# Kernel optimization log

Hardware: AMD Instinct MI355X
Metric: run time of the kernel (lower is better)

The kernel has to match this reference:

```python
import jax, jax.numpy as jnp
import numpy as np

DEPTH = 6
N_LEAF = 2 ** DEPTH          # 64
GATE_COUNT = N_LEAF - 1      # 63
IN_F = 512
OUT_F = 512
BATCH = 1024


def setup_inputs() -> dict:
    key = jax.random.key(0)
    k1, k2, k3 = jax.random.split(key, 3)
    x = jax.random.normal(k1, (BATCH, IN_F), dtype=jnp.float32)
    gw = jax.random.normal(k2, (IN_F, GATE_COUNT), dtype=jnp.float32)
    gb = jnp.zeros((GATE_COUNT,), dtype=jnp.float32)
    pw = jax.random.normal(k3, (OUT_F, IN_F, N_LEAF), dtype=jnp.float32)
    pb = jnp.zeros((OUT_F, N_LEAF), dtype=jnp.float32)
    return {"x": x, "gw": gw, "gb": gb, "pw": pw, "pb": pb}


def _leaf_probs(x, gw, gb, depth):
    # gatings: sigmoid(x @ gw + gb), shape [B, gate_count]
    g = jax.nn.sigmoid(x @ gw + gb)
    B = x.shape[0]
    dens = jnp.ones((B, 1), dtype=x.dtype)  # root density
    offset = 0
    for d in range(depth):
        n = 2 ** d
        gp = g[:, offset:offset + n]                    # parent gatings [B, n]
        # left child multiplies by g, right child by (1 - g), interleaved
        pair = jnp.stack([gp, 1.0 - gp], axis=-1).reshape(B, 2 * n)
        dens = jnp.repeat(dens, 2, axis=1) * pair        # [B, 2n]
        offset += n
    return dens  # [B, n_leaf]


def reference(x, gw, gb, pw, pb):
    leaf = _leaf_probs(x, gw, gb, DEPTH)                 # [B, L]
    # per-leaf linear projections, then mix with leaf probabilities
    y = jnp.einsum('bi,oil->bol', x, pw)                 # [B, O, L]
    out = jnp.einsum('bol,bl->bo', y, leaf) + leaf @ pb.T
    return out
```

## Files before the change

### kernel.cpp

```cpp
#include <hip/hip_runtime.h>
#include <hip/hip_bf16.h>

#define TDEPTH 6
#define NLEAF 64
#define NGATE 63
#define INF 512
#define OUTF 512
#define BATCH 1024

#define BM 256
#define BN 64
#define SPLITK 16
#define THREADS 256
#define KCH 513
#define XN 32

typedef __attribute__((ext_vector_type(4)))  float f32x4;
typedef __attribute__((ext_vector_type(16))) float f32x16;
typedef __attribute__((ext_vector_type(8)))  __bf16 bf16x8;

__global__ __launch_bounds__(256) void leaf_kernel(
    const float* __restrict__ x, const float* __restrict__ gw,
    const float* __restrict__ gb, float* __restrict__ leaf) {
  const int wid = threadIdx.x >> 6, lane = threadIdx.x & 63;
  const int b = blockIdx.x * 4 + wid;
  __shared__ float g[4][NLEAF];
  if (lane < NGATE) {
    const float* xr = x + (size_t)b * INF;
    float a0 = 0.f, a1 = 0.f, a2 = 0.f, a3 = 0.f;
    #pragma unroll 4
    for (int i = 0; i < INF; i += 4) {
      a0 += xr[i + 0] * gw[(i + 0) * NGATE + lane];
      a1 += xr[i + 1] * gw[(i + 1) * NGATE + lane];
      a2 += xr[i + 2] * gw[(i + 2) * NGATE + lane];
      a3 += xr[i + 3] * gw[(i + 3) * NGATE + lane];
    }
    float t = (a0 + a1) + (a2 + a3) + gb[lane];
    g[wid][lane] = 1.0f / (1.0f + __expf(-t));
  }
  __syncthreads();
  float p = 1.0f;
  #pragma unroll
  for (int d = 0; d < TDEPTH; d++) {
    int prefix = lane >> (TDEPTH - 1 - d);
    int node = (1 << d) - 1 + (prefix >> 1);
    float gv = g[wid][node];
    p *= (prefix & 1) ? (1.0f - gv) : gv;
  }
  leaf[(size_t)b * NLEAF + lane] = p;
}

__device__ __forceinline__ void gload_lds16(const void* g, void* l) {
  __builtin_amdgcn_global_load_lds(
      (const __attribute__((address_space(1))) void*)g,
      (__attribute__((address_space(3))) void*)l, 16, 0, 0);
}

__global__ __launch_bounds__(THREADS, 2) void gemm_kernel(
    const float* __restrict__ x, const float* __restrict__ pw,
    const float* __restrict__ pb, const float* __restrict__ leaf,
    float* __restrict__ partial) {
  __shared__ __align__(16) unsigned char Bsm[3][BN * 256];
  __shared__ __align__(16) __bf16 xsm[XN * BM];

  const int tid = threadIdx.x, lane = tid & 63, w = tid >> 6;
  const int lo = lane & 31, half = lane >> 5;

  const int L = (blockIdx.x & 7) * 64 + (blockIdx.x >> 3);
  const int mb = L & 3;
  const int rest = L >> 2;
  const int nb = rest & 7, s = rest >> 3;
  const int m0 = mb * BM, n0 = nb * BN;
  const int cs = XN * s;
  const int nreal = XN;
  const int total = XN + ((s == SPLITK - 1) ? 1 : 0);

  f32x4 lf[2][4][2];
  #pragma unroll
  for (int mr = 0; mr < 2; mr++) {
    const float* lr = leaf + (size_t)(m0 + w * 64 + mr * 32 + lo) * NLEAF + half * 8;
    #pragma unroll
    for (int t4 = 0; t4 < 4; t4++) {
      lf[mr][t4][0] = *(const f32x4*)(lr + t4 * 16);
      lf[mr][t4][1] = *(const f32x4*)(lr + t4 * 16 + 4);
    }
  }

  {
    const float* src = x + (size_t)(m0 + tid) * INF + cs;
    #pragma unroll
    for (int c4 = 0; c4 < XN / 4; c4++) {
      f32x4 v = *(const f32x4*)(src + c4 * 4);
      #pragma unroll
      for (int j = 0; j < 4; j++)
        xsm[(c4 * 4 + j) * BM + tid] = (__bf16)v[j];
    }
  }

  const int lq = lane >> 4;
  const unsigned cb = (unsigned)(lane & 15) * 16;
  unsigned pwoff[4];
  #pragma unroll
  for (int j = 0; j < 4; j++) {
    int r = w * 16 + j * 4 + lq;
    pwoff[j] = (unsigned)(n0 + r) * (unsigned)(INF * NLEAF * 4) +
               (cb ^ ((unsigned)(r & 7) << 4));
  }
  const char* pwc = (const char*)pw;
  const char* pbc = (const char*)pb;

  auto stage = [&](char* dstb_, int t) {
    char* dstb = dstb_ + w * 4096;
    const int i = cs + t;
    if (i < INF) {
      const char* srcb = pwc + (size_t)i * 256;
      #pragma unroll
      for (int j = 0; j < 4; j++) gload_lds16(srcb + pwoff[j], dstb + j * 1024);
    } else {
      #pragma unroll
      for (int j = 0; j < 4; j++) {
        int r = w * 16 + j * 4 + lq;
        unsigned o = (unsigned)(n0 + r) * (unsigned)(NLEAF * 4) +
                     (cb ^ ((unsigned)(r & 7) << 4));
        gload_lds16(pbc + o, dstb + j * 1024);
      }
    }
  };

  f32x16 acc00 = (f32x16)(0.f), acc01 = (f32x16)(0.f);
  f32x16 acc10 = (f32x16)(0.f), acc11 = (f32x16)(0.f);
  const unsigned swz = (unsigned)(lo & 7) << 4;

  auto do_step = [&](const char* bufc, int t) {
    float xv0, xv1;
    if (t < nreal) {
      xv0 = (float)xsm[t * BM + w * 64 + lo];
      xv1 = (float)xsm[t * BM + w * 64 + 32 + lo];
    } else {
      xv0 = 1.0f; xv1 = 1.0f;
    }
    #pragma unroll
    for (int t4 = 0; t4 < 4; t4++) {
      const unsigned kb = (unsigned)(t4 * 64 + half * 32);
      f32x4 b0a = *(const f32x4*)(bufc + lo * 256 + ((kb) ^ swz));
      f32x4 b0b = *(const f32x4*)(bufc + lo * 256 + ((kb + 16) ^ swz));
      f32x4 b1a = *(const f32x4*)(bufc + (32 + lo) * 256 + ((kb) ^ swz));
      f32x4 b1b = *(const f32x4*)(bufc + (32 + lo) * 256 + ((kb + 16) ^ swz));
      bf16x8 bf0, bf1;
      bf0[0] = (__bf16)b0a[0]; bf0[1] = (__bf16)b0a[1];
      bf0[2] = (__bf16)b0a[2]; bf0[3] = (__bf16)b0a[3];
      bf0[4] = (__bf16)b0b[0]; bf0[5] = (__bf16)b0b[1];
      bf0[6] = (__bf16)b0b[2]; bf0[7] = (__bf16)b0b[3];
      bf1[0] = (__bf16)b1a[0]; bf1[1] = (__bf16)b1a[1];
      bf1[2] = (__bf16)b1a[2]; bf1[3] = (__bf16)b1a[3];
      bf1[4] = (__bf16)b1b[0]; bf1[5] = (__bf16)b1b[1];
      bf1[6] = (__bf16)b1b[2]; bf1[7] = (__bf16)b1b[3];

      f32x4 p0a = lf[0][t4][0] * xv0, p0b = lf[0][t4][1] * xv0;
      f32x4 p1a = lf[1][t4][0] * xv1, p1b = lf[1][t4][1] * xv1;
      bf16x8 a0, a1;
      a0[0] = (__bf16)p0a[0]; a0[1] = (__bf16)p0a[1];
      a0[2] = (__bf16)p0a[2]; a0[3] = (__bf16)p0a[3];
      a0[4] = (__bf16)p0b[0]; a0[5] = (__bf16)p0b[1];
      a0[6] = (__bf16)p0b[2]; a0[7] = (__bf16)p0b[3];
      a1[0] = (__bf16)p1a[0]; a1[1] = (__bf16)p1a[1];
      a1[2] = (__bf16)p1a[2]; a1[3] = (__bf16)p1a[3];
      a1[4] = (__bf16)p1b[0]; a1[5] = (__bf16)p1b[1];
      a1[6] = (__bf16)p1b[2]; a1[7] = (__bf16)p1b[3];

      acc00 = __builtin_amdgcn_mfma_f32_32x32x16_bf16(a0, bf0, acc00, 0, 0, 0);
      acc01 = __builtin_amdgcn_mfma_f32_32x32x16_bf16(a0, bf1, acc01, 0, 0, 0);
      acc10 = __builtin_amdgcn_mfma_f32_32x32x16_bf16(a1, bf0, acc10, 0, 0, 0);
      acc11 = __builtin_amdgcn_mfma_f32_32x32x16_bf16(a1, bf1, acc11, 0, 0, 0);
    }
  };

  char* bA = (char*)&Bsm[0][0];
  char* bB = (char*)&Bsm[1][0];
  char* bC = (char*)&Bsm[2][0];

  stage(bA, 0);
  stage(bB, 1);
  __builtin_amdgcn_sched_barrier(0);
  asm volatile("s_waitcnt vmcnt(4) lgkmcnt(0)" ::: "memory");
  __builtin_amdgcn_s_barrier();
  __builtin_amdgcn_sched_barrier(0);

  for (int t = 0; t < total - 2; ++t) {
    stage(bC, t + 2);
    do_step(bA, t);
    __builtin_amdgcn_sched_barrier(0);
    asm volatile("s_waitcnt vmcnt(4)" ::: "memory");
    __builtin_amdgcn_s_barrier();
    __builtin_amdgcn_sched_barrier(0);
    char* tmp = bA; bA = bB; bB = bC; bC = tmp;
  }
  do_step(bA, total - 2);
  __builtin_amdgcn_sched_barrier(0);
  asm volatile("s_waitcnt vmcnt(0)" ::: "memory");
  __builtin_amdgcn_s_barrier();
  __builtin_amdgcn_sched_barrier(0);
  do_step(bB, total - 1);

  float* dst = partial + ((size_t)s * BATCH + m0 + w * 64) * OUTF + n0;
  #pragma unroll
  for (int e = 0; e < 16; e++) {
    int row = (e & 3) + 8 * (e >> 2) + 4 * half;
    dst[(size_t)row * OUTF + lo] = acc00[e];
    dst[(size_t)row * OUTF + 32 + lo] = acc01[e];
    dst[(size_t)(row + 32) * OUTF + lo] = acc10[e];
    dst[(size_t)(row + 32) * OUTF + 32 + lo] = acc11[e];
  }
}

__global__ __launch_bounds__(256) void reduce_kernel(
    const float* __restrict__ partial, float* __restrict__ out) {
  size_t e = ((size_t)blockIdx.x * 256 + threadIdx.x) * 4;
  f32x4 sum = (f32x4){0.f, 0.f, 0.f, 0.f};
  #pragma unroll
  for (int s = 0; s < SPLITK; s++)
    sum += *(const f32x4*)(partial + (size_t)s * BATCH * OUTF + e);
  *(f32x4*)(out + e) = sum;
}

extern "C" void kernel_launch(void* const* d_in, const int* in_sizes, int n_in,
                              void* d_out, int out_size, void* d_ws, size_t ws_size,
                              hipStream_t stream) {
  const float* x  = (const float*)d_in[0];
  const float* gw = (const float*)d_in[1];
  const float* gb = (const float*)d_in[2];
  const float* pw = (const float*)d_in[3];
  const float* pb = (const float*)d_in[4];
  float* out = (float*)d_out;

  float* leaf    = (float*)d_ws;
  float* partial = (float*)((char*)d_ws + (1 << 20));

  leaf_kernel<<<BATCH / 4, 256, 0, stream>>>(x, gw, gb, leaf);
  gemm_kernel<<<4 * 8 * SPLITK, THREADS, 0, stream>>>(x, pw, pb, leaf, partial);
  reduce_kernel<<<(BATCH * OUTF) / (256 * 4), 256, 0, stream>>>(partial, out);
}
```

Measured before the change: 72.27 us.

## Halve GEMM M-tile, double-buffer B stage, and raise occupancy to four blocks

The batch tile shrinks from 256 to 128 rows, so each wave computes a 32x64 tile with two MFMA accumulators instead of four, and the grid doubles to 1024 blocks. The triple-buffered LDS ring with vmcnt(4) becomes a double buffer that waits for vmcnt(0) every step. The LDS row layout and XOR swizzle are reworked to a 16-way pattern, and launch bounds ask for four blocks per CU. More blocks and higher occupancy are meant to hide latency better, but every pw tile is now loaded twice as often, which doubles B traffic, and the full drain each step serialises load and compute within a block.

```diff
diff --git a/kernel.cpp b/kernel.cpp
--- a/kernel.cpp
+++ b/kernel.cpp
@@ -8,7 +8,7 @@
 #define OUTF 512
 #define BATCH 1024
 
-#define BM 256
+#define BM 128
 #define BN 64
 #define SPLITK 16
 #define THREADS 256
@@ -56,89 +56,78 @@
       (__attribute__((address_space(3))) void*)l, 16, 0, 0);
 }
 
-__global__ __launch_bounds__(THREADS, 2) void gemm_kernel(
+__global__ __launch_bounds__(THREADS, 4) void gemm_kernel(
     const float* __restrict__ x, const float* __restrict__ pw,
     const float* __restrict__ pb, const float* __restrict__ leaf,
     float* __restrict__ partial) {
-  __shared__ __align__(16) unsigned char Bsm[3][BN * 256];
+  __shared__ __align__(16) unsigned char Bsm[2][BN * 256];
   __shared__ __align__(16) __bf16 xsm[XN * BM];
 
   const int tid = threadIdx.x, lane = tid & 63, w = tid >> 6;
   const int lo = lane & 31, half = lane >> 5;
 
-  const int L = (blockIdx.x & 7) * 64 + (blockIdx.x >> 3);
-  const int mb = L & 3;
-  const int rest = L >> 2;
+  const int L = (blockIdx.x & 7) * 128 + (blockIdx.x >> 3);
+  const int mb = L & 7;
+  const int rest = L >> 3;
   const int nb = rest & 7, s = rest >> 3;
   const int m0 = mb * BM, n0 = nb * BN;
   const int cs = XN * s;
-  const int nreal = XN;
   const int total = XN + ((s == SPLITK - 1) ? 1 : 0);
 
-  f32x4 lf[2][4][2];
-  #pragma unroll
-  for (int mr = 0; mr < 2; mr++) {
-    const float* lr = leaf + (size_t)(m0 + w * 64 + mr * 32 + lo) * NLEAF + half * 8;
+  f32x4 lf[4][2];
+  {
+    const float* lr = leaf + (size_t)(m0 + w * 32 + lo) * NLEAF + half * 8;
     #pragma unroll
     for (int t4 = 0; t4 < 4; t4++) {
-      lf[mr][t4][0] = *(const f32x4*)(lr + t4 * 16);
-      lf[mr][t4][1] = *(const f32x4*)(lr + t4 * 16 + 4);
+      lf[t4][0] = *(const f32x4*)(lr + t4 * 16);
+      lf[t4][1] = *(const f32x4*)(lr + t4 * 16 + 4);
     }
   }
 
   {
-    const float* src = x + (size_t)(m0 + tid) * INF + cs;
+    const int row = tid >> 1, h = tid & 1;
+    const float* src = x + (size_t)(m0 + row) * INF + cs + h * 16;
     #pragma unroll
-    for (int c4 = 0; c4 < XN / 4; c4++) {
+    for (int c4 = 0; c4 < 4; c4++) {
       f32x4 v = *(const f32x4*)(src + c4 * 4);
       #pragma unroll
       for (int j = 0; j < 4; j++)
-        xsm[(c4 * 4 + j) * BM + tid] = (__bf16)v[j];
+        xsm[(h * 16 + c4 * 4 + j) * BM + row] = (__bf16)v[j];
     }
   }
 
   const int lq = lane >> 4;
-  const unsigned cb = (unsigned)(lane & 15) * 16;
-  unsigned pwoff[4];
+  const unsigned cg = (unsigned)(lane & 15);
+  const unsigned gsw = (cg ^ ((unsigned)(4 * w + lq) & 15)) * 16;
+  unsigned pwoff[4], pboff[4];
   #pragma unroll
   for (int j = 0; j < 4; j++) {
-    int r = w * 16 + j * 4 + lq;
-    pwoff[j] = (unsigned)(n0 + r) * (unsigned)(INF * NLEAF * 4) +
-               (cb ^ ((unsigned)(r & 7) << 4));
+    int r = j * 16 + 4 * w + lq;
+    pwoff[j] = (unsigned)(n0 + r) * (unsigned)(INF * NLEAF * 4) + gsw;
+    pboff[j] = (unsigned)(n0 + r) * (unsigned)(NLEAF * 4) + gsw;
   }
   const char* pwc = (const char*)pw;
   const char* pbc = (const char*)pb;
 
-  auto stage = [&](char* dstb_, int t) {
-    char* dstb = dstb_ + w * 4096;
+  auto stage = [&](char* dstb, int t) {
     const int i = cs + t;
     if (i < INF) {
       const char* srcb = pwc + (size_t)i * 256;
       #pragma unroll
-      for (int j = 0; j < 4; j++) gload_lds16(srcb + pwoff[j], dstb + j * 1024);
+      for (int j = 0; j < 4; j++)
+        gload_lds16(srcb + pwoff[j], dstb + (j * 16 + 4 * w) * 256);
     } else {
       #pragma unroll
-      for (int j = 0; j < 4; j++) {
-        int r = w * 16 + j * 4 + lq;
-        unsigned o = (unsigned)(n0 + r) * (unsigned)(NLEAF * 4) +
-                     (cb ^ ((unsigned)(r & 7) << 4));
-        gload_lds16(pbc + o, dstb + j * 1024);
-      }
+      for (int j = 0; j < 4; j++)
+        gload_lds16(pbc + pboff[j], dstb + (j * 16 + 4 * w) * 256);
     }
   };
 
-  f32x16 acc00 = (f32x16)(0.f), acc01 = (f32x16)(0.f);
-  f32x16 acc10 = (f32x16)(0.f), acc11 = (f32x16)(0.f);
-  const unsigned swz = (unsigned)(lo & 7) << 4;
+  f32x16 acc0 = (f32x16)(0.f), acc1 = (f32x16)(0.f);
+  const unsigned swz = (unsigned)(lo & 15) << 4;
 
   auto do_step = [&](const char* bufc, int t) {
-    float xv0, xv1;
-    if (t < nreal) {
-      xv0 = (float)xsm[t * BM + w * 64 + lo];
-      xv1 = (float)xsm[t * BM + w * 64 + 32 + lo];
-    } else {
-      xv0 = 1.0f; xv1 = 1.0f;
-    }
+    const float xv = (t < XN) ? (float)xsm[t * BM + w * 32 + lo] : 1.0f;
     #pragma unroll
     for (int t4 = 0; t4 < 4; t4++) {
       const unsigned kb = (unsigned)(t4 * 64 + half * 32);
@@ -156,60 +145,43 @@
       bf1[4] = (__bf16)b1b[0]; bf1[5] = (__bf16)b1b[1];
       bf1[6] = (__bf16)b1b[2]; bf1[7] = (__bf16)b1b[3];
 
-      f32x4 p0a = lf[0][t4][0] * xv0, p0b = lf[0][t4][1] * xv0;
-      f32x4 p1a = lf[1][t4][0] * xv1, p1b = lf[1][t4][1] * xv1;
-      bf16x8 a0, a1;
-      a0[0] = (__bf16)p0a[0]; a0[1] = (__bf16)p0a[1];
-      a0[2] = (__bf16)p0a[2]; a0[3] = (__bf16)p0a[3];
-      a0[4] = (__bf16)p0b[0]; a0[5] = (__bf16)p0b[1];
-      a0[6] = (__bf16)p0b[2]; a0[7] = (__bf16)p0b[3];
-      a1[0] = (__bf16)p1a[0]; a1[1] = (__bf16)p1a[1];
-      a1[2] = (__bf16)p1a[2]; a1[3] = (__bf16)p1a[3];
-      a1[4] = (__bf16)p1b[0]; a1[5] = (__bf16)p1b[1];
-      a1[6] = (__bf16)p1b[2]; a1[7] = (__bf16)p1b[3];
-
-      acc00 = __builtin_amdgcn_mfma_f32_32x32x16_bf16(a0, bf0, acc00, 0, 0, 0);
-      acc01 = __builtin_amdgcn_mfma_f32_32x32x16_bf16(a0, bf1, acc01, 0, 0, 0);
-      acc10 = __builtin_amdgcn_mfma_f32_32x32x16_bf16(a1, bf0, acc10, 0, 0, 0);
-      acc11 = __builtin_amdgcn_mfma_f32_32x32x16_bf16(a1, bf1, acc11, 0, 0, 0);
+      f32x4 pa = lf[t4][0] * xv, pbv = lf[t4][1] * xv;
+      bf16x8 a;
+      a[0] = (__bf16)pa[0]; a[1] = (__bf16)pa[1];
+      a[2] = (__bf16)pa[2]; a[3] = (__bf16)pa[3];
+      a[4] = (__bf16)pbv[0]; a[5] = (__bf16)pbv[1];
+      a[6] = (__bf16)pbv[2]; a[7] = (__bf16)pbv[3];
+
+      acc0 = __builtin_amdgcn_mfma_f32_32x32x16_bf16(a, bf0, acc0, 0, 0, 0);
+      acc1 = __builtin_amdgcn_mfma_f32_32x32x16_bf16(a, bf1, acc1, 0, 0, 0);
     }
   };
 
   char* bA = (char*)&Bsm[0][0];
   char* bB = (char*)&Bsm[1][0];
-  char* bC = (char*)&Bsm[2][0];
 
   stage(bA, 0);
-  stage(bB, 1);
   __builtin_amdgcn_sched_barrier(0);
-  asm volatile("s_waitcnt vmcnt(4) lgkmcnt(0)" ::: "memory");
+  asm volatile("s_waitcnt vmcnt(0) lgkmcnt(0)" ::: "memory");
   __builtin_amdgcn_s_barrier();
   __builtin_amdgcn_sched_barrier(0);
 
-  for (int t = 0; t < total - 2; ++t) {
-    stage(bC, t + 2);
+  for (int t = 0; t < total; ++t) {
+    if (t + 1 < total) stage(bB, t + 1);
     do_step(bA, t);
     __builtin_amdgcn_sched_barrier(0);
-    asm volatile("s_waitcnt vmcnt(4)" ::: "memory");
+    asm volatile("s_waitcnt vmcnt(0)" ::: "memory");
     __builtin_amdgcn_s_barrier();
     __builtin_amdgcn_sched_barrier(0);
-    char* tmp = bA; bA = bB; bB = bC; bC = tmp;
-  }
-  do_step(bA, total - 2);
-  __builtin_amdgcn_sched_barrier(0);
-  asm volatile("s_waitcnt vmcnt(0)" ::: "memory");
-  __builtin_amdgcn_s_barrier();
-  __builtin_amdgcn_sched_barrier(0);
-  do_step(bB, total - 1);
-
-  float* dst = partial + ((size_t)s * BATCH + m0 + w * 64) * OUTF + n0;
+    char* tmp = bA; bA = bB; bB = tmp;
+  }
+
+  float* dst = partial + ((size_t)s * BATCH + m0 + w * 32) * OUTF + n0;
   #pragma unroll
   for (int e = 0; e < 16; e++) {
     int row = (e & 3) + 8 * (e >> 2) + 4 * half;
-    dst[(size_t)row * OUTF + lo] = acc00[e];
-    dst[(size_t)row * OUTF + 32 + lo] = acc01[e];
-    dst[(size_t)(row + 32) * OUTF + lo] = acc10[e];
-    dst[(size_t)(row + 32) * OUTF + 32 + lo] = acc11[e];
+    dst[(size_t)row * OUTF + lo] = acc0[e];
+    dst[(size_t)row * OUTF + 32 + lo] = acc1[e];
   }
 }
 
@@ -237,6 +209,6 @@
   float* partial = (float*)((char*)d_ws + (1 << 20));
 
   leaf_kernel<<<BATCH / 4, 256, 0, stream>>>(x, gw, gb, leaf);
-  gemm_kernel<<<4 * 8 * SPLITK, THREADS, 0, stream>>>(x, pw, pb, leaf, partial);
+  gemm_kernel<<<8 * 8 * SPLITK, THREADS, 0, stream>>>(x, pw, pb, leaf, partial);
   reduce_kernel<<<(BATCH * OUTF) / (256 * 4), 256, 0, stream>>>(partial, out);
 }
```

Result: slower. 77.43 us (+7.1%).

## Pre-convert pw to swizzled bf16 in prep kernel and fold bias into epilogue

Applied to the files above, without the earlier changes.

A prep kernel now computes the leaf probabilities and also converts the full pw tensor to bf16 in a pre-swizzled layout, so the GEMM streams half the bytes per stage and drops the per-step fp32-to-bf16 conversion of B. The pb bias term moves out of the K loop into an epilogue MFMA on the last split. The split-K count becomes a template parameter selected by workspace size. In exchange, every call pays an extra full read of pw in fp32 plus a bf16 write, which may cost more traffic than it saves.

```diff
diff --git a/kernel.cpp b/kernel.cpp
--- a/kernel.cpp
+++ b/kernel.cpp
@@ -10,44 +10,64 @@
 
 #define BM 256
 #define BN 64
-#define SPLITK 16
 #define THREADS 256
-#define KCH 513
-#define XN 32
 
 typedef __attribute__((ext_vector_type(4)))  float f32x4;
 typedef __attribute__((ext_vector_type(16))) float f32x16;
 typedef __attribute__((ext_vector_type(8)))  __bf16 bf16x8;
 
-__global__ __launch_bounds__(256) void leaf_kernel(
+__device__ __forceinline__ bf16x8 pack8(f32x4 a, f32x4 b) {
+  bf16x8 w;
+  w[0] = (__bf16)a[0]; w[1] = (__bf16)a[1];
+  w[2] = (__bf16)a[2]; w[3] = (__bf16)a[3];
+  w[4] = (__bf16)b[0]; w[5] = (__bf16)b[1];
+  w[6] = (__bf16)b[2]; w[7] = (__bf16)b[3];
+  return w;
+}
+
+__global__ __launch_bounds__(256) void prep_kernel(
     const float* __restrict__ x, const float* __restrict__ gw,
-    const float* __restrict__ gb, float* __restrict__ leaf) {
-  const int wid = threadIdx.x >> 6, lane = threadIdx.x & 63;
-  const int b = blockIdx.x * 4 + wid;
-  __shared__ float g[4][NLEAF];
-  if (lane < NGATE) {
-    const float* xr = x + (size_t)b * INF;
-    float a0 = 0.f, a1 = 0.f, a2 = 0.f, a3 = 0.f;
-    #pragma unroll 4
-    for (int i = 0; i < INF; i += 4) {
-      a0 += xr[i + 0] * gw[(i + 0) * NGATE + lane];
-      a1 += xr[i + 1] * gw[(i + 1) * NGATE + lane];
-      a2 += xr[i + 2] * gw[(i + 2) * NGATE + lane];
-      a3 += xr[i + 3] * gw[(i + 3) * NGATE + lane];
-    }
-    float t = (a0 + a1) + (a2 + a3) + gb[lane];
-    g[wid][lane] = 1.0f / (1.0f + __expf(-t));
-  }
-  __syncthreads();
-  float p = 1.0f;
-  #pragma unroll
-  for (int d = 0; d < TDEPTH; d++) {
-    int prefix = lane >> (TDEPTH - 1 - d);
-    int node = (1 << d) - 1 + (prefix >> 1);
-    float gv = g[wid][node];
-    p *= (prefix & 1) ? (1.0f - gv) : gv;
-  }
-  leaf[(size_t)b * NLEAF + lane] = p;
+    const float* __restrict__ gb, const float* __restrict__ pw,
+    float* __restrict__ leaf, __bf16* __restrict__ pwb) {
+  const int tid = threadIdx.x;
+  if (blockIdx.x < 256) {
+    const int wid = tid >> 6, lane = tid & 63;
+    const int b = blockIdx.x * 4 + wid;
+    __shared__ float g[4][NLEAF];
+    if (lane < NGATE) {
+      const float* xr = x + (size_t)b * INF;
+      float a0 = 0.f, a1 = 0.f, a2 = 0.f, a3 = 0.f;
+      #pragma unroll 4
+      for (int i = 0; i < INF; i += 4) {
+        a0 += xr[i + 0] * gw[(i + 0) * NGATE + lane];
+        a1 += xr[i + 1] * gw[(i + 1) * NGATE + lane];
+        a2 += xr[i + 2] * gw[(i + 2) * NGATE + lane];
+        a3 += xr[i + 3] * gw[(i + 3) * NGATE + lane];
+      }
+      float t = (a0 + a1) + (a2 + a3) + gb[lane];
+      g[wid][lane] = 1.0f / (1.0f + __expf(-t));
+    }
+    __syncthreads();
+    float p = 1.0f;
+    #pragma unroll
+    for (int d = 0; d < TDEPTH; d++) {
+      int prefix = lane >> (TDEPTH - 1 - d);
+      int node = (1 << d) - 1 + (prefix >> 1);
+      float gv = g[wid][node];
+      p *= (prefix & 1) ? (1.0f - gv) : gv;
+    }
+    leaf[(size_t)b * NLEAF + lane] = p;
+  } else {
+    const unsigned G = (blockIdx.x - 256) * 256 + tid;
+    const unsigned o = G >> 12, rem = G & 4095;
+    const unsigned ipair = rem >> 4, p = rem & 15;
+    const unsigned g = p ^ (o & 15);
+    const unsigned i = ipair * 2 + (g >> 3), kg = g & 7;
+    const float* src = pw + (((size_t)o * INF + i) * NLEAF + kg * 8);
+    f32x4 a = *(const f32x4*)src, b = *(const f32x4*)(src + 4);
+    *(bf16x8*)((char*)pwb + (((size_t)o << 16) + (ipair << 8) + (p << 4))) =
+        pack8(a, b);
+  }
 }
 
 __device__ __forceinline__ void gload_lds16(const void* g, void* l) {
@@ -56,122 +76,92 @@
       (__attribute__((address_space(3))) void*)l, 16, 0, 0);
 }
 
+template <int S>
 __global__ __launch_bounds__(THREADS, 2) void gemm_kernel(
-    const float* __restrict__ x, const float* __restrict__ pw,
-    const float* __restrict__ pb, const float* __restrict__ leaf,
+    const __bf16* __restrict__ pwb, const float* __restrict__ pb,
+    const float* __restrict__ x, const float* __restrict__ leaf,
     float* __restrict__ partial) {
-  __shared__ __align__(16) unsigned char Bsm[3][BN * 256];
-  __shared__ __align__(16) __bf16 xsm[XN * BM];
+  constexpr int NSTEP = 256 / S;
+  constexpr int NPL = 512 / S;
+  __shared__ __align__(16) __bf16 Bsm[3][BN * 128];
+  __shared__ __align__(16) __bf16 xsm[NPL][BM];
 
   const int tid = threadIdx.x, lane = tid & 63, w = tid >> 6;
   const int lo = lane & 31, half = lane >> 5;
 
-  const int L = (blockIdx.x & 7) * 64 + (blockIdx.x >> 3);
+  const int nwg = 4 * 8 * S;
+  const int L = (blockIdx.x & 7) * (nwg / 8) + (blockIdx.x >> 3);
   const int mb = L & 3;
   const int rest = L >> 2;
   const int nb = rest & 7, s = rest >> 3;
   const int m0 = mb * BM, n0 = nb * BN;
-  const int cs = XN * s;
-  const int nreal = XN;
-  const int total = XN + ((s == SPLITK - 1) ? 1 : 0);
+  const int ip0 = s * NSTEP;
+  const int cs = s * NPL;
 
   f32x4 lf[2][4][2];
   #pragma unroll
-  for (int mr = 0; mr < 2; mr++) {
-    const float* lr = leaf + (size_t)(m0 + w * 64 + mr * 32 + lo) * NLEAF + half * 8;
+  for (int mt = 0; mt < 2; mt++) {
+    const float* lr =
+        leaf + (size_t)(m0 + w * 64 + mt * 32 + lo) * NLEAF + half * 8;
     #pragma unroll
     for (int t4 = 0; t4 < 4; t4++) {
-      lf[mr][t4][0] = *(const f32x4*)(lr + t4 * 16);
-      lf[mr][t4][1] = *(const f32x4*)(lr + t4 * 16 + 4);
+      lf[mt][t4][0] = *(const f32x4*)(lr + t4 * 16);
+      lf[mt][t4][1] = *(const f32x4*)(lr + t4 * 16 + 4);
     }
   }
 
   {
     const float* src = x + (size_t)(m0 + tid) * INF + cs;
     #pragma unroll
-    for (int c4 = 0; c4 < XN / 4; c4++) {
+    for (int c4 = 0; c4 < NPL / 4; c4++) {
       f32x4 v = *(const f32x4*)(src + c4 * 4);
       #pragma unroll
-      for (int j = 0; j < 4; j++)
-        xsm[(c4 * 4 + j) * BM + tid] = (__bf16)v[j];
-    }
-  }
-
-  const int lq = lane >> 4;
-  const unsigned cb = (unsigned)(lane & 15) * 16;
-  unsigned pwoff[4];
+      for (int j = 0; j < 4; j++) xsm[c4 * 4 + j][tid] = (__bf16)v[j];
+    }
+  }
+
+  size_t pwoff[4];
   #pragma unroll
   for (int j = 0; j < 4; j++) {
-    int r = w * 16 + j * 4 + lq;
-    pwoff[j] = (unsigned)(n0 + r) * (unsigned)(INF * NLEAF * 4) +
-               (cb ^ ((unsigned)(r & 7) << 4));
-  }
-  const char* pwc = (const char*)pw;
-  const char* pbc = (const char*)pb;
-
-  auto stage = [&](char* dstb_, int t) {
-    char* dstb = dstb_ + w * 4096;
-    const int i = cs + t;
-    if (i < INF) {
-      const char* srcb = pwc + (size_t)i * 256;
-      #pragma unroll
-      for (int j = 0; j < 4; j++) gload_lds16(srcb + pwoff[j], dstb + j * 1024);
-    } else {
-      #pragma unroll
-      for (int j = 0; j < 4; j++) {
-        int r = w * 16 + j * 4 + lq;
-        unsigned o = (unsigned)(n0 + r) * (unsigned)(NLEAF * 4) +
-                     (cb ^ ((unsigned)(r & 7) << 4));
-        gload_lds16(pbc + o, dstb + j * 1024);
-      }
-    }
+    int r = j * 16 + w * 4 + (lane >> 4);
+    pwoff[j] = ((size_t)(n0 + r) << 16) + ((unsigned)(lane & 15) << 4);
+  }
+  const char* pwc = (const char*)pwb;
+
+  auto stage = [&](char* dstb, int t) {
+    const char* srcb = pwc + ((size_t)(ip0 + t) << 8);
+    #pragma unroll
+    for (int j = 0; j < 4; j++)
+      gload_lds16(srcb + pwoff[j], dstb + j * 4096 + w * 1024);
   };
 
   f32x16 acc00 = (f32x16)(0.f), acc01 = (f32x16)(0.f);
   f32x16 acc10 = (f32x16)(0.f), acc11 = (f32x16)(0.f);
-  const unsigned swz = (unsigned)(lo & 7) << 4;
+  const unsigned swz = (unsigned)(lo & 15) << 4;
 
   auto do_step = [&](const char* bufc, int t) {
-    float xv0, xv1;
-    if (t < nreal) {
-      xv0 = (float)xsm[t * BM + w * 64 + lo];
-      xv1 = (float)xsm[t * BM + w * 64 + 32 + lo];
-    } else {
-      xv0 = 1.0f; xv1 = 1.0f;
-    }
-    #pragma unroll
-    for (int t4 = 0; t4 < 4; t4++) {
-      const unsigned kb = (unsigned)(t4 * 64 + half * 32);
-      f32x4 b0a = *(const f32x4*)(bufc + lo * 256 + ((kb) ^ swz));
-      f32x4 b0b = *(const f32x4*)(bufc + lo * 256 + ((kb + 16) ^ swz));
-      f32x4 b1a = *(const f32x4*)(bufc + (32 + lo) * 256 + ((kb) ^ swz));
-      f32x4 b1b = *(const f32x4*)(bufc + (32 + lo) * 256 + ((kb + 16) ^ swz));
-      bf16x8 bf0, bf1;
-      bf0[0] = (__bf16)b0a[0]; bf0[1] = (__bf16)b0a[1];
-      bf0[2] = (__bf16)b0a[2]; bf0[3] = (__bf16)b0a[3];
-      bf0[4] = (__bf16)b0b[0]; bf0[5] = (__bf16)b0b[1];
-      bf0[6] = (__bf16)b0b[2]; bf0[7] = (__bf16)b0b[3];
-      bf1[0] = (__bf16)b1a[0]; bf1[1] = (__bf16)b1a[1];
-      bf1[2] = (__bf16)b1a[2]; bf1[3] = (__bf16)b1a[3];
-      bf1[4] = (__bf16)b1b[0]; bf1[5] = (__bf16)b1b[1];
-      bf1[6] = (__bf16)b1b[2]; bf1[7] = (__bf16)b1b[3];
-
-      f32x4 p0a = lf[0][t4][0] * xv0, p0b = lf[0][t4][1] * xv0;
-      f32x4 p1a = lf[1][t4][0] * xv1, p1b = lf[1][t4][1] * xv1;
-      bf16x8 a0, a1;
-      a0[0] = (__bf16)p0a[0]; a0[1] = (__bf16)p0a[1];
-      a0[2] = (__bf16)p0a[2]; a0[3] = (__bf16)p0a[3];
-      a0[4] = (__bf16)p0b[0]; a0[5] = (__bf16)p0b[1];
-      a0[6] = (__bf16)p0b[2]; a0[7] = (__bf16)p0b[3];
-      a1[0] = (__bf16)p1a[0]; a1[1] = (__bf16)p1a[1];
-      a1[2] = (__bf16)p1a[2]; a1[3] = (__bf16)p1a[3];
-      a1[4] = (__bf16)p1b[0]; a1[5] = (__bf16)p1b[1];
-      a1[6] = (__bf16)p1b[2]; a1[7] = (__bf16)p1b[3];
-
-      acc00 = __builtin_amdgcn_mfma_f32_32x32x16_bf16(a0, bf0, acc00, 0, 0, 0);
-      acc01 = __builtin_amdgcn_mfma_f32_32x32x16_bf16(a0, bf1, acc01, 0, 0, 0);
-      acc10 = __builtin_amdgcn_mfma_f32_32x32x16_bf16(a1, bf0, acc10, 0, 0, 0);
-      acc11 = __builtin_amdgcn_mfma_f32_32x32x16_bf16(a1, bf1, acc11, 0, 0, 0);
+    const float xv00 = (float)xsm[2 * t][w * 64 + lo];
+    const float xv01 = (float)xsm[2 * t + 1][w * 64 + lo];
+    const float xv10 = (float)xsm[2 * t][w * 64 + 32 + lo];
+    const float xv11 = (float)xsm[2 * t + 1][w * 64 + 32 + lo];
+    #pragma unroll
+    for (int pl = 0; pl < 2; pl++) {
+      const float x0 = pl ? xv01 : xv00;
+      const float x1 = pl ? xv11 : xv10;
+      #pragma unroll
+      for (int t4 = 0; t4 < 4; t4++) {
+        const unsigned kb = ((unsigned)(pl * 128 + t4 * 32 + half * 16)) ^ swz;
+        bf16x8 bf0 = *(const bf16x8*)(bufc + lo * 256 + kb);
+        bf16x8 bf1 = *(const bf16x8*)(bufc + (32 + lo) * 256 + kb);
+        f32x4 p0a = lf[0][t4][0] * x0, p0b = lf[0][t4][1] * x0;
+        f32x4 p1a = lf[1][t4][0] * x1, p1b = lf[1][t4][1] * x1;
+        bf16x8 a0 = pack8(p0a, p0b);
+        bf16x8 a1 = pack8(p1a, p1b);
+        acc00 = __builtin_amdgcn_mfma_f32_32x32x16_bf16(a0, bf0, acc00, 0, 0, 0);
+        acc01 = __builtin_amdgcn_mfma_f32_32x32x16_bf16(a0, bf1, acc01, 0, 0, 0);
+        acc10 = __builtin_amdgcn_mfma_f32_32x32x16_bf16(a1, bf0, acc10, 0, 0, 0);
+        acc11 = __builtin_amdgcn_mfma_f32_32x32x16_bf16(a1, bf1, acc11, 0, 0, 0);
+      }
     }
   };
 
@@ -182,43 +172,73 @@
   stage(bA, 0);
   stage(bB, 1);
   __builtin_amdgcn_sched_barrier(0);
-  asm volatile("s_waitcnt vmcnt(4) lgkmcnt(0)" ::: "memory");
+  asm volatile("s_waitcnt vmcnt(0) lgkmcnt(0)" ::: "memory");
   __builtin_amdgcn_s_barrier();
   __builtin_amdgcn_sched_barrier(0);
 
-  for (int t = 0; t < total - 2; ++t) {
+  for (int t = 0; t < NSTEP - 2; ++t) {
     stage(bC, t + 2);
     do_step(bA, t);
     __builtin_amdgcn_sched_barrier(0);
-    asm volatile("s_waitcnt vmcnt(4)" ::: "memory");
+    asm volatile("s_waitcnt vmcnt(4) lgkmcnt(0)" ::: "memory");
     __builtin_amdgcn_s_barrier();
     __builtin_amdgcn_sched_barrier(0);
     char* tmp = bA; bA = bB; bB = bC; bC = tmp;
   }
-  do_step(bA, total - 2);
-  __builtin_amdgcn_sched_barrier(0);
-  asm volatile("s_waitcnt vmcnt(0)" ::: "memory");
+  do_step(bA, NSTEP - 2);
+  __builtin_amdgcn_sched_barrier(0);
+  asm volatile("s_waitcnt vmcnt(0) lgkmcnt(0)" ::: "memory");
   __builtin_amdgcn_s_barrier();
   __builtin_amdgcn_sched_barrier(0);
-  do_step(bB, total - 1);
-
-  float* dst = partial + ((size_t)s * BATCH + m0 + w * 64) * OUTF + n0;
-  #pragma unroll
-  for (int e = 0; e < 16; e++) {
-    int row = (e & 3) + 8 * (e >> 2) + 4 * half;
-    dst[(size_t)row * OUTF + lo] = acc00[e];
-    dst[(size_t)row * OUTF + 32 + lo] = acc01[e];
-    dst[(size_t)(row + 32) * OUTF + lo] = acc10[e];
-    dst[(size_t)(row + 32) * OUTF + 32 + lo] = acc11[e];
-  }
-}
-
+  do_step(bB, NSTEP - 1);
+
+  if (s == S - 1) {
+    #pragma unroll
+    for (int t4 = 0; t4 < 4; t4++) {
+      bf16x8 a0 = pack8(lf[0][t4][0], lf[0][t4][1]);
+      bf16x8 a1 = pack8(lf[1][t4][0], lf[1][t4][1]);
+      #pragma unroll
+      for (int nt = 0; nt < 2; nt++) {
+        const float* pr =
+            pb + (size_t)(n0 + nt * 32 + lo) * NLEAF + t4 * 16 + half * 8;
+        f32x4 c0 = *(const f32x4*)pr, c1 = *(const f32x4*)(pr + 4);
+        bf16x8 bb = pack8(c0, c1);
+        if (nt == 0) {
+          acc00 = __builtin_amdgcn_mfma_f32_32x32x16_bf16(a0, bb, acc00, 0, 0, 0);
+          acc10 = __builtin_amdgcn_mfma_f32_32x32x16_bf16(a1, bb, acc10, 0, 0, 0);
+        } else {
+          acc01 = __builtin_amdgcn_mfma_f32_32x32x16_bf16(a0, bb, acc01, 0, 0, 0);
+          acc11 = __builtin_amdgcn_mfma_f32_32x32x16_bf16(a1, bb, acc11, 0, 0, 0);
+        }
+      }
+    }
+  }
+
+  #pragma unroll
+  for (int mt = 0; mt < 2; mt++) {
+    float* dst =
+        partial + ((size_t)s * BATCH + m0 + w * 64 + mt * 32) * OUTF + n0;
+    #pragma unroll
+    for (int e = 0; e < 16; e++) {
+      int row = (e & 3) + 8 * (e >> 2) + 4 * half;
+      if (mt == 0) {
+        dst[(size_t)row * OUTF + lo] = acc00[e];
+        dst[(size_t)row * OUTF + 32 + lo] = acc01[e];
+      } else {
+        dst[(size_t)row * OUTF + lo] = acc10[e];
+        dst[(size_t)row * OUTF + 32 + lo] = acc11[e];
+      }
+    }
+  }
+}
+
+template <int S>
 __global__ __launch_bounds__(256) void reduce_kernel(
     const float* __restrict__ partial, float* __restrict__ out) {
   size_t e = ((size_t)blockIdx.x * 256 + threadIdx.x) * 4;
   f32x4 sum = (f32x4){0.f, 0.f, 0.f, 0.f};
   #pragma unroll
-  for (int s = 0; s < SPLITK; s++)
+  for (int s = 0; s < S; s++)
     sum += *(const f32x4*)(partial + (size_t)s * BATCH * OUTF + e);
   *(f32x4*)(out + e) = sum;
 }
@@ -233,10 +253,18 @@
   const float* pb = (const float*)d_in[4];
   float* out = (float*)d_out;
 
-  float* leaf    = (float*)d_ws;
-  float* partial = (float*)((char*)d_ws + (1 << 20));
-
-  leaf_kernel<<<BATCH / 4, 256, 0, stream>>>(x, gw, gb, leaf);
-  gemm_kernel<<<4 * 8 * SPLITK, THREADS, 0, stream>>>(x, pw, pb, leaf, partial);
-  reduce_kernel<<<(BATCH * OUTF) / (256 * 4), 256, 0, stream>>>(partial, out);
-}
+  float*  leaf    = (float*)d_ws;
+  __bf16* pwb     = (__bf16*)((char*)d_ws + (1 << 20));
+  float*  partial = (float*)((char*)d_ws + (33ull << 20));
+
+  prep_kernel<<<256 + 8192, 256, 0, stream>>>(x, gw, gb, pw, leaf, pwb);
+
+  const size_t need16 = (33ull << 20) + (size_t)16 * BATCH * OUTF * 4;
+  if (ws_size >= need16) {
+    gemm_kernel<16><<<4 * 8 * 16, THREADS, 0, stream>>>(pwb, pb, x, leaf, partial);
+    reduce_kernel<16><<<(BATCH * OUTF) / (256 * 4), 256, 0, stream>>>(partial, out);
+  } else {
+    gemm_kernel<8><<<4 * 8 * 8, THREADS, 0, stream>>>(pwb, pb, x, leaf, partial);
+    reduce_kernel<8><<<(BATCH * OUTF) / (256 * 4), 256, 0, stream>>>(partial, out);
+  }
+}
```

After: 70.48 us. 2.5% less time.
